# Kernel tuning notes

Hardware: AMD Instinct MI355X
Metric: run time of the kernel (lower is better)

Reference implementation:

```python
import jax, jax.numpy as jnp
import numpy as np

EPS = 1e-06  # matches SQRegularizer eps


def setup_inputs() -> dict:
    key = jax.random.key(0)
    k1, k2, k3, k4 = jax.random.split(key, 4)
    B, P, S, N = 8, 16, 256, 4096
    surface_points = jax.random.normal(k1, (B, P, S, 3), dtype=jnp.float32)
    points = jax.random.normal(k2, (B, N, 3), dtype=jnp.float32)
    assign_matrix = jax.random.uniform(k3, (B, N, P), dtype=jnp.float32)
    exist = jax.random.uniform(k4, (B, P), dtype=jnp.float32)
    return {
        "surface_points": surface_points,
        "points": points,
        "assign_matrix": assign_matrix,
        "exist": exist,
    }


def reference(surface_points, points, assign_matrix, exist):
    # Squared pairwise distances via ||a||^2 + ||b||^2 - 2 a.b  (== cdist(...)**2)
    a2 = jnp.sum(surface_points * surface_points, axis=-1)          # (B, P, S)
    b2 = jnp.sum(points * points, axis=-1)                          # (B, N)
    cross = jnp.einsum('bpsd,bnd->bpsn', surface_points, points)    # (B, P, S, N)
    d2 = jnp.maximum(a2[..., None] + b2[:, None, None, :] - 2.0 * cross, 0.0)

    # point -> superquadric: min over samples, weighted by soft assignment
    p2s = jnp.min(d2, axis=2)                                       # (B, P, N)
    p2s = jnp.transpose(p2s, (0, 2, 1))                             # (B, N, P)
    point_to_sq = jnp.mean(jnp.mean(jnp.sum(p2s * assign_matrix, axis=-1), axis=-1))

    # superquadric -> point: min over points, mean over samples, existence-weighted
    s2p = jnp.mean(jnp.min(d2, axis=3), axis=-1)                    # (B, P)
    denom = jnp.maximum(jnp.sum(exist, axis=-1), EPS)               # (B,)
    sq_to_point = jnp.mean(jnp.sum(s2p * exist, axis=-1) / denom)

    return point_to_sq + sq_to_point
```

## Files before the change

kernel.cpp:

```cpp
#include <hip/hip_runtime.h>

#define NB 8
#define NP 16
#define NS 256
#define NN 4096
#define NBP (NB*NP)
#define NCHUNK 8
#define CHUNK (NN/NCHUNK)
#define NBLK (NBP*NCHUNK)
#define EPSV 1e-6f

typedef _Float16 half8 __attribute__((ext_vector_type(8)));
typedef float    f32x4 __attribute__((ext_vector_type(4)));

#define H0 ((_Float16)0.0f)
#define H1 ((_Float16)1.0f)



__global__ __launch_bounds__(256) void sqreg_main(
    const float* __restrict__ sp,
    const float* __restrict__ pts,
    const float* __restrict__ assign,
    float* __restrict__ minw,
    float* __restrict__ partials)
{
    __shared__ __align__(16) _Float16 lsa[NS][16];
    __shared__ __align__(16) _Float16 lpb[CHUNK][16];
    __shared__ float pm1[4][CHUNK];
    __shared__ float psum[4];

    const int bid   = blockIdx.x;
    const int bp    = bid >> 3;
    const int chunk = bid & 7;
    const int p     = bp & 15;
    const int b     = bp >> 4;
    const int tid   = threadIdx.x;
    const int lane  = tid & 63;
    const int wave  = tid >> 6;
    const int l15   = lane & 15;
    const int lg    = lane >> 4;

    {
        const float* s3 = sp + (size_t)(bp*NS)*3;
        float x = s3[tid*3+0], y = s3[tid*3+1], z = s3[tid*3+2];
        float a2 = x*x + y*y + z*z;
        _Float16 xh=(_Float16)x, yh=(_Float16)y, zh=(_Float16)z, ah=(_Float16)a2;
        _Float16 xl=(_Float16)(x-(float)xh), yl=(_Float16)(y-(float)yh);
        _Float16 zl=(_Float16)(z-(float)zh), al=(_Float16)(a2-(float)ah);
        half8 lo = {xh,xh,xl,yh,yh,yl,zh,zh};
        half8 hi = {zl,ah,al,H1,H1,H0,H0,H0};
        *(half8*)&lsa[tid][0] = lo;
        *(half8*)&lsa[tid][8] = hi;

        const float* q3 = pts + (size_t)(b*NN + chunk*CHUNK)*3;
#pragma unroll
        for (int k = 0; k < 2; ++k) {
            int i = tid + k*256;
            float bx = q3[i*3+0], by = q3[i*3+1], bz = q3[i*3+2];
            float tx = -2.0f*bx, ty = -2.0f*by, tz = -2.0f*bz;
            float b2 = bx*bx + by*by + bz*bz;
            _Float16 txh=(_Float16)tx, tyh=(_Float16)ty, tzh=(_Float16)tz, bh=(_Float16)b2;
            _Float16 txl=(_Float16)(tx-(float)txh), tyl=(_Float16)(ty-(float)tyh);
            _Float16 tzl=(_Float16)(tz-(float)tzh), bl=(_Float16)(b2-(float)bh);
            half8 blo = {txh,txl,txh,tyh,tyl,tyh,tzh,tzl};
            half8 bhi = {tzh,H1,H1,bh,bl,H0,H0,H0};
            *(half8*)&lpb[i][0] = blo;
            *(half8*)&lpb[i][8] = bhi;
        }
    }
    __syncthreads();

    half8 afrag[4];
#pragma unroll
    for (int st = 0; st < 4; ++st) {
        half8 t = {H0,H0,H0,H0,H0,H0,H0,H0};
        if (lane < 32)
            t = *(const half8*)&lsa[wave*64 + st*16 + l15][(lane>>4)*8];
        afrag[st] = t;
    }

    f32x4 rmin[4];
#pragma unroll
    for (int st = 0; st < 4; ++st)
        rmin[st] = (f32x4){INFINITY, INFINITY, INFINITY, INFINITY};

#pragma unroll 2
    for (int nt = 0; nt < 32; ++nt) {
        half8 bf = {H0,H0,H0,H0,H0,H0,H0,H0};
        if (lane < 32)
            bf = *(const half8*)&lpb[nt*16 + l15][(lane>>4)*8];

        f32x4 acc[4];
#pragma unroll
        for (int st = 0; st < 4; ++st)
            acc[st] = __builtin_amdgcn_mfma_f32_16x16x32_f16(
                afrag[st], bf, (f32x4){0.f,0.f,0.f,0.f}, 0, 0, 0);

        float cm = INFINITY;
#pragma unroll
        for (int st = 0; st < 4; ++st) {
            rmin[st][0] = fminf(rmin[st][0], acc[st][0]);
            rmin[st][1] = fminf(rmin[st][1], acc[st][1]);
            rmin[st][2] = fminf(rmin[st][2], acc[st][2]);
            rmin[st][3] = fminf(rmin[st][3], acc[st][3]);
            cm = fminf(cm, fminf(fminf(acc[st][0], acc[st][1]),
                                 fminf(acc[st][2], acc[st][3])));
        }
        cm = fminf(cm, __shfl_xor(cm, 16, 64));
        cm = fminf(cm, __shfl_xor(cm, 32, 64));
        if (lane < 16) pm1[wave][nt*16 + lane] = cm;
    }

#pragma unroll
    for (int st = 0; st < 4; ++st) {
#pragma unroll
        for (int r = 0; r < 4; ++r) {
            float v = rmin[st][r];
            v = fminf(v, __shfl_xor(v, 1, 64));
            v = fminf(v, __shfl_xor(v, 2, 64));
            v = fminf(v, __shfl_xor(v, 4, 64));
            v = fminf(v, __shfl_xor(v, 8, 64));
            if (l15 == 0)
                minw[(size_t)bid*NS + wave*64 + st*16 + lg*4 + r] = fmaxf(v, 0.0f);
        }
    }
    __syncthreads();

    float acc = 0.0f;
#pragma unroll
    for (int j = 0; j < 2; ++j) {
        int n = tid + j*256;
        float mm = fminf(fminf(pm1[0][n], pm1[1][n]),
                         fminf(pm1[2][n], pm1[3][n]));
        float d  = fmaxf(mm, 0.0f);
        acc += d * assign[(size_t)(b*NN + chunk*CHUNK + n)*NP + p];
    }
#pragma unroll
    for (int msk = 32; msk >= 1; msk >>= 1)
        acc += __shfl_xor(acc, msk, 64);
    if (lane == 0) psum[wave] = acc;
    __syncthreads();
    if (tid == 0) partials[bid] = psum[0] + psum[1] + psum[2] + psum[3];
}

__global__ __launch_bounds__(256) void sqreg_tail(
    const float* __restrict__ minw,
    const float* __restrict__ partials,
    float* __restrict__ s2p,
    float* __restrict__ pp)
{
    __shared__ float wsum[4];
    const int bp   = blockIdx.x;
    const int tid  = threadIdx.x;
    const int lane = tid & 63;
    const int wave = tid >> 6;

    const float* base = minw + (size_t)(bp*NCHUNK)*NS + tid;
    float m = base[0];
#pragma unroll
    for (int c = 1; c < NCHUNK; ++c) m = fminf(m, base[(size_t)c*NS]);
#pragma unroll
    for (int msk = 32; msk >= 1; msk >>= 1)
        m += __shfl_xor(m, msk, 64);
    if (lane == 0) wsum[wave] = m;
    __syncthreads();

    if (tid == 0) {
        s2p[bp] = (wsum[0] + wsum[1] + wsum[2] + wsum[3]) * (1.0f/(float)NS);
        float a = 0.0f;
#pragma unroll
        for (int c = 0; c < NCHUNK; ++c) a += partials[bp*NCHUNK + c];
        pp[bp] = a;
    }
}

__global__ __launch_bounds__(256) void sqreg_final(
    const float* __restrict__ s2p,
    const float* __restrict__ pp,
    const float* __restrict__ exist,
    float* __restrict__ out)
{
    __shared__ float ppw[2];
    __shared__ float fin[8];
    const int tid = threadIdx.x;

    float tsum = (tid < NBP) ? pp[tid] : 0.0f;
#pragma unroll
    for (int msk = 32; msk >= 1; msk >>= 1)
        tsum += __shfl_xor(tsum, msk, 64);
    if (tid == 0)  ppw[0] = tsum;
    if (tid == 64) ppw[1] = tsum;

    if (tid < NBP) {
        float e  = exist[tid];
        float sv = s2p[tid] * e;
#pragma unroll
        for (int msk = 8; msk >= 1; msk >>= 1) {
            e  += __shfl_xor(e,  msk, 64);
            sv += __shfl_xor(sv, msk, 64);
        }
        if ((tid & 15) == 0) fin[tid >> 4] = sv / fmaxf(e, EPSV);
    }
    __syncthreads();

    if (tid == 0) {
        float sq = 0.0f;
#pragma unroll
        for (int g = 0; g < NB; ++g) sq += fin[g];
        out[0] = (ppw[0] + ppw[1]) / (float)(NB*NN) + sq * (1.0f/(float)NB);
    }
}

extern "C" void kernel_launch(void* const* d_in, const int* in_sizes, int n_in,
                              void* d_out, int out_size, void* d_ws, size_t ws_size,
                              hipStream_t stream) {
    const float* sp     = (const float*)d_in[0];
    const float* pts    = (const float*)d_in[1];
    const float* assign = (const float*)d_in[2];
    const float* exist  = (const float*)d_in[3];
    float* out = (float*)d_out;

    char* ws = (char*)d_ws;
    float* minw = (float*)(ws);
    float* part = (float*)(ws + 0x100000);
    float* s2p  = (float*)(ws + 0x101000);
    float* pp   = (float*)(ws + 0x101200);

    sqreg_main <<<NBLK, 256, 0, stream>>>(sp, pts, assign, minw, part);
    sqreg_tail <<<NBP,  256, 0, stream>>>(minw, part, s2p, pp);
    sqreg_final<<<1,    256, 0, stream>>>(s2p, pp, exist, out);
}
```

Before: 28.95 us.

## Switch distance MFMA from 16x16x32 to 32x32x16 tiles

Replaces the four 16x16x32 f16 MFMAs per point tile with two 32x32x16 MFMAs covering 32 samples by 32 points. The 16-wide K dimension now fits the packed split-precision operands, so all 64 lanes carry useful data instead of half being zero-padded. This halves the number of LDS B loads and loop iterations and reduces shuffle work per point column. In exchange it needs more accumulator registers (two 16-wide vectors plus min state), may lower occupancy, and the row-min reduction gains an extra shuffle stage.

```diff
diff --git a/kernel.cpp b/kernel.cpp
--- a/kernel.cpp
+++ b/kernel.cpp
@@ -10,8 +10,8 @@
 #define NBLK (NBP*NCHUNK)
 #define EPSV 1e-6f
 
-typedef _Float16 half8 __attribute__((ext_vector_type(8)));
-typedef float    f32x4 __attribute__((ext_vector_type(4)));
+typedef _Float16 half8  __attribute__((ext_vector_type(8)));
+typedef float    f32x16 __attribute__((ext_vector_type(16)));
 
 #define H0 ((_Float16)0.0f)
 #define H1 ((_Float16)1.0f)
@@ -38,8 +38,8 @@
     const int tid   = threadIdx.x;
     const int lane  = tid & 63;
     const int wave  = tid >> 6;
-    const int l15   = lane & 15;
-    const int lg    = lane >> 4;
+    const int l31   = lane & 31;
+    const int hi    = lane >> 5;
 
     {
         const float* s3 = sp + (size_t)(bp*NS)*3;
@@ -49,9 +49,9 @@
         _Float16 xl=(_Float16)(x-(float)xh), yl=(_Float16)(y-(float)yh);
         _Float16 zl=(_Float16)(z-(float)zh), al=(_Float16)(a2-(float)ah);
         half8 lo = {xh,xh,xl,yh,yh,yl,zh,zh};
-        half8 hi = {zl,ah,al,H1,H1,H0,H0,H0};
+        half8 hi8 = {zl,ah,al,H1,H1,H0,H0,H0};
         *(half8*)&lsa[tid][0] = lo;
-        *(half8*)&lsa[tid][8] = hi;
+        *(half8*)&lsa[tid][8] = hi8;
 
         const float* q3 = pts + (size_t)(b*NN + chunk*CHUNK)*3;
 #pragma unroll
@@ -71,58 +71,48 @@
     }
     __syncthreads();
 
-    half8 afrag[4];
-#pragma unroll
-    for (int st = 0; st < 4; ++st) {
-        half8 t = {H0,H0,H0,H0,H0,H0,H0,H0};
-        if (lane < 32)
-            t = *(const half8*)&lsa[wave*64 + st*16 + l15][(lane>>4)*8];
-        afrag[st] = t;
-    }
-
-    f32x4 rmin[4];
-#pragma unroll
-    for (int st = 0; st < 4; ++st)
-        rmin[st] = (f32x4){INFINITY, INFINITY, INFINITY, INFINITY};
-
-#pragma unroll 2
-    for (int nt = 0; nt < 32; ++nt) {
-        half8 bf = {H0,H0,H0,H0,H0,H0,H0,H0};
-        if (lane < 32)
-            bf = *(const half8*)&lpb[nt*16 + l15][(lane>>4)*8];
-
-        f32x4 acc[4];
-#pragma unroll
-        for (int st = 0; st < 4; ++st)
-            acc[st] = __builtin_amdgcn_mfma_f32_16x16x32_f16(
-                afrag[st], bf, (f32x4){0.f,0.f,0.f,0.f}, 0, 0, 0);
+    half8 afrag[2];
+#pragma unroll
+    for (int st = 0; st < 2; ++st)
+        afrag[st] = *(const half8*)&lsa[wave*64 + st*32 + l31][hi*8];
+
+    f32x16 rmin0, rmin1;
+#pragma unroll
+    for (int r = 0; r < 16; ++r) { rmin0[r] = INFINITY; rmin1[r] = INFINITY; }
+
+    for (int nt = 0; nt < 16; ++nt) {
+        half8 bf = *(const half8*)&lpb[nt*32 + l31][hi*8];
+
+        f32x16 a0 = __builtin_amdgcn_mfma_f32_32x32x16_f16(afrag[0], bf,
+                        (f32x16)(0.0f), 0, 0, 0);
+        f32x16 a1 = __builtin_amdgcn_mfma_f32_32x32x16_f16(afrag[1], bf,
+                        (f32x16)(0.0f), 0, 0, 0);
 
         float cm = INFINITY;
 #pragma unroll
-        for (int st = 0; st < 4; ++st) {
-            rmin[st][0] = fminf(rmin[st][0], acc[st][0]);
-            rmin[st][1] = fminf(rmin[st][1], acc[st][1]);
-            rmin[st][2] = fminf(rmin[st][2], acc[st][2]);
-            rmin[st][3] = fminf(rmin[st][3], acc[st][3]);
-            cm = fminf(cm, fminf(fminf(acc[st][0], acc[st][1]),
-                                 fminf(acc[st][2], acc[st][3])));
-        }
-        cm = fminf(cm, __shfl_xor(cm, 16, 64));
+        for (int r = 0; r < 16; ++r) {
+            rmin0[r] = fminf(rmin0[r], a0[r]);
+            rmin1[r] = fminf(rmin1[r], a1[r]);
+            cm = fminf(cm, fminf(a0[r], a1[r]));
+        }
         cm = fminf(cm, __shfl_xor(cm, 32, 64));
-        if (lane < 16) pm1[wave][nt*16 + lane] = cm;
-    }
-
-#pragma unroll
-    for (int st = 0; st < 4; ++st) {
-#pragma unroll
-        for (int r = 0; r < 4; ++r) {
-            float v = rmin[st][r];
+        pm1[wave][nt*32 + l31] = cm;
+    }
+
+#pragma unroll
+    for (int st = 0; st < 2; ++st) {
+#pragma unroll
+        for (int r = 0; r < 16; ++r) {
+            float v = (st == 0) ? rmin0[r] : rmin1[r];
             v = fminf(v, __shfl_xor(v, 1, 64));
             v = fminf(v, __shfl_xor(v, 2, 64));
             v = fminf(v, __shfl_xor(v, 4, 64));
             v = fminf(v, __shfl_xor(v, 8, 64));
-            if (l15 == 0)
-                minw[(size_t)bid*NS + wave*64 + st*16 + lg*4 + r] = fmaxf(v, 0.0f);
+            v = fminf(v, __shfl_xor(v, 16, 64));
+            if (l31 == 0) {
+                int s = wave*64 + st*32 + (r & 3) + 8*(r >> 2) + 4*hi;
+                minw[(size_t)bid*NS + s] = fmaxf(v, 0.0f);
+            }
         }
     }
     __syncthreads();
```

Result: slower. 35.69 us (+23.3%).

## Split points into 16 chunks and swap MFMA operand roles per wave

Applied to the files above, without the earlier changes.

Doubles the number of point chunks so the main kernel launches 2048 blocks of 256 points each instead of 1024 blocks of 512, adding occupancy hints via launch bounds. Each wave now holds 64 points as the stationary MFMA operand and streams all 256 surface samples, keeping per-point minima in registers and per-sample minima reduced through shared memory. This aims to fill the GPU better and shorten per-block latency, at the cost of more surface-sample setup work per block, more partial rows for the tail kernel to reduce, and a larger workspace.

```diff
diff --git a/kernel.cpp b/kernel.cpp
--- a/kernel.cpp
+++ b/kernel.cpp
@@ -5,7 +5,7 @@
 #define NS 256
 #define NN 4096
 #define NBP (NB*NP)
-#define NCHUNK 8
+#define NCHUNK 16
 #define CHUNK (NN/NCHUNK)
 #define NBLK (NBP*NCHUNK)
 #define EPSV 1e-6f
@@ -18,7 +18,7 @@
 
 
 
-__global__ __launch_bounds__(256) void sqreg_main(
+__global__ __launch_bounds__(256, 4) void sqreg_main(
     const float* __restrict__ sp,
     const float* __restrict__ pts,
     const float* __restrict__ assign,
@@ -27,19 +27,19 @@
 {
     __shared__ __align__(16) _Float16 lsa[NS][16];
     __shared__ __align__(16) _Float16 lpb[CHUNK][16];
-    __shared__ float pm1[4][CHUNK];
+    __shared__ float pm1[CHUNK];
+    __shared__ float pm2[4][NS];
     __shared__ float psum[4];
 
     const int bid   = blockIdx.x;
-    const int bp    = bid >> 3;
-    const int chunk = bid & 7;
+    const int bp    = bid >> 4;
+    const int chunk = bid & 15;
     const int p     = bp & 15;
     const int b     = bp >> 4;
     const int tid   = threadIdx.x;
     const int lane  = tid & 63;
     const int wave  = tid >> 6;
     const int l15   = lane & 15;
-    const int lg    = lane >> 4;
 
     {
         const float* s3 = sp + (size_t)(bp*NS)*3;
@@ -48,98 +48,103 @@
         _Float16 xh=(_Float16)x, yh=(_Float16)y, zh=(_Float16)z, ah=(_Float16)a2;
         _Float16 xl=(_Float16)(x-(float)xh), yl=(_Float16)(y-(float)yh);
         _Float16 zl=(_Float16)(z-(float)zh), al=(_Float16)(a2-(float)ah);
-        half8 lo = {xh,xh,xl,yh,yh,yl,zh,zh};
-        half8 hi = {zl,ah,al,H1,H1,H0,H0,H0};
-        *(half8*)&lsa[tid][0] = lo;
-        *(half8*)&lsa[tid][8] = hi;
+        half8 blo = {xh,xh,xl,yh,yh,yl,zh,zh};
+        half8 bhi = {zl,ah,al,H1,H1,H0,H0,H0};
+        *(half8*)&lsa[tid][0] = blo;
+        *(half8*)&lsa[tid][8] = bhi;
 
         const float* q3 = pts + (size_t)(b*NN + chunk*CHUNK)*3;
-#pragma unroll
-        for (int k = 0; k < 2; ++k) {
-            int i = tid + k*256;
-            float bx = q3[i*3+0], by = q3[i*3+1], bz = q3[i*3+2];
-            float tx = -2.0f*bx, ty = -2.0f*by, tz = -2.0f*bz;
-            float b2 = bx*bx + by*by + bz*bz;
-            _Float16 txh=(_Float16)tx, tyh=(_Float16)ty, tzh=(_Float16)tz, bh=(_Float16)b2;
-            _Float16 txl=(_Float16)(tx-(float)txh), tyl=(_Float16)(ty-(float)tyh);
-            _Float16 tzl=(_Float16)(tz-(float)tzh), bl=(_Float16)(b2-(float)bh);
-            half8 blo = {txh,txl,txh,tyh,tyl,tyh,tzh,tzl};
-            half8 bhi = {tzh,H1,H1,bh,bl,H0,H0,H0};
-            *(half8*)&lpb[i][0] = blo;
-            *(half8*)&lpb[i][8] = bhi;
-        }
+        float bx = q3[tid*3+0], by = q3[tid*3+1], bz = q3[tid*3+2];
+        float tx = -2.0f*bx, ty = -2.0f*by, tz = -2.0f*bz;
+        float b2 = bx*bx + by*by + bz*bz;
+        _Float16 txh=(_Float16)tx, tyh=(_Float16)ty, tzh=(_Float16)tz, bh=(_Float16)b2;
+        _Float16 txl=(_Float16)(tx-(float)txh), tyl=(_Float16)(ty-(float)tyh);
+        _Float16 tzl=(_Float16)(tz-(float)tzh), bl=(_Float16)(b2-(float)bh);
+        half8 alo = {txh,txl,txh,tyh,tyl,tyh,tzh,tzl};
+        half8 ahi = {tzh,H1,H1,bh,bl,H0,H0,H0};
+        *(half8*)&lpb[tid][0] = alo;
+        *(half8*)&lpb[tid][8] = ahi;
     }
     __syncthreads();
 
     half8 afrag[4];
 #pragma unroll
-    for (int st = 0; st < 4; ++st) {
+    for (int j = 0; j < 4; ++j) {
         half8 t = {H0,H0,H0,H0,H0,H0,H0,H0};
         if (lane < 32)
-            t = *(const half8*)&lsa[wave*64 + st*16 + l15][(lane>>4)*8];
-        afrag[st] = t;
-    }
-
-    f32x4 rmin[4];
-#pragma unroll
-    for (int st = 0; st < 4; ++st)
-        rmin[st] = (f32x4){INFINITY, INFINITY, INFINITY, INFINITY};
-
-#pragma unroll 2
-    for (int nt = 0; nt < 32; ++nt) {
+            t = *(const half8*)&lpb[wave*64 + j*16 + l15][(lane>>4)*8];
+        afrag[j] = t;
+    }
+
+    f32x4 rp1[4];
+#pragma unroll
+    for (int j = 0; j < 4; ++j) rp1[j] = (f32x4){INFINITY,INFINITY,INFINITY,INFINITY};
+    float rp2[16];
+#pragma unroll
+    for (int st = 0; st < 16; ++st) rp2[st] = INFINITY;
+
+#pragma unroll 4
+    for (int st = 0; st < 16; ++st) {
         half8 bf = {H0,H0,H0,H0,H0,H0,H0,H0};
         if (lane < 32)
-            bf = *(const half8*)&lpb[nt*16 + l15][(lane>>4)*8];
+            bf = *(const half8*)&lsa[st*16 + l15][(lane>>4)*8];
 
         f32x4 acc[4];
 #pragma unroll
-        for (int st = 0; st < 4; ++st)
-            acc[st] = __builtin_amdgcn_mfma_f32_16x16x32_f16(
-                afrag[st], bf, (f32x4){0.f,0.f,0.f,0.f}, 0, 0, 0);
-
-        float cm = INFINITY;
-#pragma unroll
-        for (int st = 0; st < 4; ++st) {
-            rmin[st][0] = fminf(rmin[st][0], acc[st][0]);
-            rmin[st][1] = fminf(rmin[st][1], acc[st][1]);
-            rmin[st][2] = fminf(rmin[st][2], acc[st][2]);
-            rmin[st][3] = fminf(rmin[st][3], acc[st][3]);
-            cm = fminf(cm, fminf(fminf(acc[st][0], acc[st][1]),
-                                 fminf(acc[st][2], acc[st][3])));
+        for (int j = 0; j < 4; ++j)
+            acc[j] = __builtin_amdgcn_mfma_f32_16x16x32_f16(
+                afrag[j], bf, (f32x4){0.f,0.f,0.f,0.f}, 0, 0, 0);
+
+        float t0, t1;
+#pragma unroll
+        for (int j = 0; j < 4; ++j) {
+            rp1[j][0] = fminf(rp1[j][0], acc[j][0]);
+            rp1[j][1] = fminf(rp1[j][1], acc[j][1]);
+            rp1[j][2] = fminf(rp1[j][2], acc[j][2]);
+            rp1[j][3] = fminf(rp1[j][3], acc[j][3]);
         }
-        cm = fminf(cm, __shfl_xor(cm, 16, 64));
-        cm = fminf(cm, __shfl_xor(cm, 32, 64));
-        if (lane < 16) pm1[wave][nt*16 + lane] = cm;
-    }
-
-#pragma unroll
-    for (int st = 0; st < 4; ++st) {
+        t0 = fminf(fminf(acc[0][0], acc[0][1]), fminf(acc[0][2], acc[0][3]));
+        t1 = fminf(fminf(acc[1][0], acc[1][1]), fminf(acc[1][2], acc[1][3]));
+        t0 = fminf(t0, t1);
+        t1 = fminf(fminf(acc[2][0], acc[2][1]), fminf(acc[2][2], acc[2][3]));
+        t0 = fminf(t0, t1);
+        t1 = fminf(fminf(acc[3][0], acc[3][1]), fminf(acc[3][2], acc[3][3]));
+        rp2[st] = fminf(rp2[st], fminf(t0, t1));
+    }
+
+#pragma unroll
+    for (int st = 0; st < 16; ++st) {
+        float v = rp2[st];
+        v = fminf(v, __shfl_xor(v, 16, 64));
+        v = fminf(v, __shfl_xor(v, 32, 64));
+        pm2[wave][st*16 + l15] = v;
+    }
+
+#pragma unroll
+    for (int j = 0; j < 4; ++j) {
 #pragma unroll
         for (int r = 0; r < 4; ++r) {
-            float v = rmin[st][r];
+            float v = rp1[j][r];
             v = fminf(v, __shfl_xor(v, 1, 64));
             v = fminf(v, __shfl_xor(v, 2, 64));
             v = fminf(v, __shfl_xor(v, 4, 64));
             v = fminf(v, __shfl_xor(v, 8, 64));
-            if (l15 == 0)
-                minw[(size_t)bid*NS + wave*64 + st*16 + lg*4 + r] = fmaxf(v, 0.0f);
+            pm1[wave*64 + j*16 + (lane>>4)*4 + r] = v;
         }
     }
     __syncthreads();
 
-    float acc = 0.0f;
-#pragma unroll
-    for (int j = 0; j < 2; ++j) {
-        int n = tid + j*256;
-        float mm = fminf(fminf(pm1[0][n], pm1[1][n]),
-                         fminf(pm1[2][n], pm1[3][n]));
-        float d  = fmaxf(mm, 0.0f);
-        acc += d * assign[(size_t)(b*NN + chunk*CHUNK + n)*NP + p];
-    }
+    {
+        float mm = fminf(fminf(pm2[0][tid], pm2[1][tid]),
+                         fminf(pm2[2][tid], pm2[3][tid]));
+        minw[(size_t)bid*NS + tid] = fmaxf(mm, 0.0f);
+    }
+    float acc = fmaxf(pm1[tid], 0.0f) *
+                assign[(size_t)(b*NN + chunk*CHUNK + tid)*NP + p];
 #pragma unroll
     for (int msk = 32; msk >= 1; msk >>= 1)
         acc += __shfl_xor(acc, msk, 64);
-    if (lane == 0) psum[wave] = acc;
+    if ((tid & 63) == 0) psum[wave] = acc;
     __syncthreads();
     if (tid == 0) partials[bid] = psum[0] + psum[1] + psum[2] + psum[3];
 }
@@ -223,9 +228,9 @@
 
     char* ws = (char*)d_ws;
     float* minw = (float*)(ws);
-    float* part = (float*)(ws + 0x100000);
-    float* s2p  = (float*)(ws + 0x101000);
-    float* pp   = (float*)(ws + 0x101200);
+    float* part = (float*)(ws + 0x200000);
+    float* s2p  = (float*)(ws + 0x202000);
+    float* pp   = (float*)(ws + 0x202400);
 
     sqreg_main <<<NBLK, 256, 0, stream>>>(sp, pts, assign, minw, part);
     sqreg_tail <<<NBP,  256, 0, stream>>>(minw, part, s2p, pp);
```

New measurement: 28.02 us. 3.2% less time.
